# Performance work log

Measured on AMD Instinct MI355X. Metric: run time of the kernel, lower is better.

Reference implementation:

```python
import jax, jax.numpy as jnp
import numpy as np

N_WAY = 5
N_SHOT = 10

def setup_inputs() -> dict:
    key = jax.random.key(0)
    k1, k2, k3, k4 = jax.random.split(key, 4)
    B, n_support, n_query, T, F, D = 32, 50, 75, 128, 64, 256
    support_x = jax.random.normal(k1, (B, n_support, T, F), dtype=jnp.float32)
    query_x = jax.random.normal(k2, (B, n_query, T, F), dtype=jnp.float32)
    # episodic labels: every class present exactly N_SHOT times per episode
    support_y = jnp.broadcast_to(jnp.repeat(jnp.arange(N_WAY), N_SHOT)[None, :], (B, n_support))
    W = jax.random.normal(k3, (F, D), dtype=jnp.float32) * 0.05
    b = jax.random.normal(k4, (D,), dtype=jnp.float32) * 0.05
    return {"support_x": support_x, "support_y": support_y, "query_x": query_x, "W": W, "b": b}

def _encode(x, W, b):
    # mean-pool over time, then linear projection: [B, N, T, F] -> [B, N, D]
    return jnp.einsum('bntf,fd->bnd', x, W) / x.shape[2] + b

def reference(support_x, support_y, query_x, W, b):
    B, n_query = query_x.shape[0], query_x.shape[1]
    support_z = _encode(support_x, W, b)   # [B, S, D]
    query_z = _encode(query_x, W, b)       # [B, Q, D]
    # label-grouped mean (prototypes) via one-hot segment sum, all episodes at once
    onehot = (support_y[..., None] == jnp.arange(N_WAY)).astype(support_z.dtype)  # [B, S, K]
    counts = onehot.sum(axis=1)                                                   # [B, K]
    prototypes = jnp.einsum('bsk,bsd->bkd', onehot, support_z) / counts[..., None]
    # Euclidean cdist: [B, Q, K]
    diff = query_z[:, :, None, :] - prototypes[:, None, :, :]
    dists = jnp.sqrt(jnp.sum(diff * diff, axis=-1))
    logits = -dists
    return logits.reshape(B * n_query, N_WAY)
```

## Files before the change

### kernel.cpp

```cpp
#include <hip/hip_runtime.h>
#include <math.h>

#define B_  32
#define NS_ 50
#define NQ_ 75
#define T_  128
#define F_  64
#define D_  256
#define K_  5
#define NR_ (NS_ + NQ_)
#define QT_ 25

__global__ __launch_bounds__(256) void meanpool_kernel(
    const float* __restrict__ sx, const float* __restrict__ qx,
    float* __restrict__ meanbuf)
{
    const int bid = blockIdx.x;
    const int b = bid / NR_, n = bid % NR_;
    const float* src = (n < NS_)
        ? (sx + (size_t)(b * NS_ + n) * (T_ * F_))
        : (qx + (size_t)(b * NQ_ + (n - NS_)) * (T_ * F_));
    const float4* src4 = (const float4*)src;

    const int tid = threadIdx.x;
    const int f4 = tid & 15;

    float4 acc = make_float4(0.f, 0.f, 0.f, 0.f);
    for (int t = (tid >> 4); t < T_; t += 16) {
        float4 v = src4[t * 16 + f4];
        acc.x += v.x; acc.y += v.y; acc.z += v.z; acc.w += v.w;
    }
    acc.x += __shfl_down(acc.x, 32); acc.y += __shfl_down(acc.y, 32);
    acc.z += __shfl_down(acc.z, 32); acc.w += __shfl_down(acc.w, 32);
    acc.x += __shfl_down(acc.x, 16); acc.y += __shfl_down(acc.y, 16);
    acc.z += __shfl_down(acc.z, 16); acc.w += __shfl_down(acc.w, 16);

    __shared__ float4 red[4][16];
    const int wave = tid >> 6, lane = tid & 63;
    if (lane < 16) red[wave][lane] = acc;
    __syncthreads();
    if (tid < 16) {
        float4 a = red[0][tid], b4 = red[1][tid], c = red[2][tid], d4 = red[3][tid];
        float4 s;
        s.x = (a.x + b4.x + c.x + d4.x) * (1.f / T_);
        s.y = (a.y + b4.y + c.y + d4.y) * (1.f / T_);
        s.z = (a.z + b4.z + c.z + d4.z) * (1.f / T_);
        s.w = (a.w + b4.w + c.w + d4.w) * (1.f / T_);
        ((float4*)meanbuf)[(size_t)bid * 16 + tid] = s;
    }
}

__global__ __launch_bounds__(256) void proto_kernel(
    const float* __restrict__ meanbuf, const int* __restrict__ sy,
    const float* __restrict__ Wm, const float* __restrict__ bias,
    float* __restrict__ out)
{
    __shared__ float rows[QT_ + K_][F_];
    __shared__ float zbuf[QT_ + K_][D_];
    __shared__ int   labels[NS_];
    __shared__ float psum[K_][F_];
    __shared__ int   counts[K_];

    const int tid = threadIdx.x;
    const int bid = blockIdx.x;
    const int b = bid / 3, qt = bid % 3;
    const int q0 = qt * QT_;

    if (tid < NS_) labels[tid] = sy[b * NS_ + tid];
    __syncthreads();

    if (tid < F_) {
        const int f = tid;
        float p0 = 0.f, p1 = 0.f, p2 = 0.f, p3 = 0.f, p4 = 0.f;
        for (int s = 0; s < NS_; ++s) {
            float v = meanbuf[((size_t)b * NR_ + s) * F_ + f];
            int l = labels[s];
            if      (l == 0) p0 += v;
            else if (l == 1) p1 += v;
            else if (l == 2) p2 += v;
            else if (l == 3) p3 += v;
            else             p4 += v;
        }
        psum[0][f] = p0; psum[1][f] = p1; psum[2][f] = p2;
        psum[3][f] = p3; psum[4][f] = p4;
    }
    if (tid < K_) {
        int c = 0;
        for (int s = 0; s < NS_; ++s) c += (labels[s] == tid);
        counts[tid] = c;
    }
    for (int i = tid; i < QT_ * F_; i += 256) {
        int r = i / F_, f = i % F_;
        rows[r][f] = meanbuf[((size_t)b * NR_ + NS_ + q0 + r) * F_ + f];
    }
    __syncthreads();
    for (int i = tid; i < K_ * F_; i += 256) {
        int k = i / F_, f = i % F_;
        rows[QT_ + k][f] = psum[k][f] / (float)counts[k];
    }
    __syncthreads();

    {
        const int d = tid;
        float wreg[F_];
#pragma unroll
        for (int f = 0; f < F_; ++f) wreg[f] = Wm[f * D_ + d];
        const float bd = bias[d];
        for (int r = 0; r < QT_ + K_; ++r) {
            float acc = bd;
#pragma unroll
            for (int f = 0; f < F_; ++f) acc += rows[r][f] * wreg[f];
            zbuf[r][d] = acc;
        }
    }
    __syncthreads();

    const int wave = tid >> 6, lane = tid & 63;
    for (int p = wave; p < QT_ * K_; p += 4) {
        const int q = p / K_, k = p % K_;
        float s = 0.f;
#pragma unroll
        for (int j = 0; j < 4; ++j) {
            int d = lane + j * 64;
            float diff = zbuf[q][d] - zbuf[QT_ + k][d];
            s += diff * diff;
        }
        for (int off = 32; off > 0; off >>= 1) s += __shfl_down(s, off);
        if (lane == 0) out[(size_t)(b * NQ_ + q0 + q) * K_ + k] = -sqrtf(s);
    }
}

extern "C" void kernel_launch(void* const* d_in, const int* in_sizes, int n_in,
                              void* d_out, int out_size, void* d_ws, size_t ws_size,
                              hipStream_t stream) {
    const float* sx   = (const float*)d_in[0];
    const int*   sy   = (const int*)  d_in[1];
    const float* qx   = (const float*)d_in[2];
    const float* Wm   = (const float*)d_in[3];
    const float* bias = (const float*)d_in[4];
    float* out = (float*)d_out;
    float* meanbuf = (float*)d_ws;

    meanpool_kernel<<<B_ * NR_, 256, 0, stream>>>(sx, qx, meanbuf);
    proto_kernel<<<B_ * 3, 256, 0, stream>>>(meanbuf, sy, Wm, bias, out);
}
```

Measured before the change: 202.8 us.

## Fuse linear projection into mean-pool kernel and simplify distance kernel

Moves the F-to-D projection out of the small 96-block second kernel and into the 4000-block mean-pool kernel, so each encoded row is projected once right after pooling. The second kernel now only builds prototypes from projected support rows and computes distances. The time loop is also fully unrolled. In exchange, every pooling block loads the full 64-float weight column per thread, which adds register pressure and weight reads, and the workspace grows from D=64 to D=256 floats per row.

```diff
diff --git a/kernel.cpp b/kernel.cpp
--- a/kernel.cpp
+++ b/kernel.cpp
@@ -11,9 +11,10 @@
 #define NR_ (NS_ + NQ_)
 #define QT_ 25
 
-__global__ __launch_bounds__(256) void meanpool_kernel(
+__global__ __launch_bounds__(256) void encode_kernel(
     const float* __restrict__ sx, const float* __restrict__ qx,
-    float* __restrict__ meanbuf)
+    const float* __restrict__ Wm, const float* __restrict__ bias,
+    float* __restrict__ zbuf)
 {
     const int bid = blockIdx.x;
     const int b = bid / NR_, n = bid % NR_;
@@ -23,10 +24,17 @@
     const float4* src4 = (const float4*)src;
 
     const int tid = threadIdx.x;
+
+    float wreg[F_];
+#pragma unroll
+    for (int f = 0; f < F_; ++f) wreg[f] = Wm[f * D_ + tid];
+    const float bd = bias[tid];
+
     const int f4 = tid & 15;
-
     float4 acc = make_float4(0.f, 0.f, 0.f, 0.f);
-    for (int t = (tid >> 4); t < T_; t += 16) {
+#pragma unroll
+    for (int j = 0; j < 8; ++j) {
+        int t = (tid >> 4) + j * 16;
         float4 v = src4[t * 16 + f4];
         acc.x += v.x; acc.y += v.y; acc.z += v.z; acc.w += v.w;
     }
@@ -36,6 +44,7 @@
     acc.z += __shfl_down(acc.z, 16); acc.w += __shfl_down(acc.w, 16);
 
     __shared__ float4 red[4][16];
+    __shared__ float  mean[F_];
     const int wave = tid >> 6, lane = tid & 63;
     if (lane < 16) red[wave][lane] = acc;
     __syncthreads();
@@ -46,20 +55,27 @@
         s.y = (a.y + b4.y + c.y + d4.y) * (1.f / T_);
         s.z = (a.z + b4.z + c.z + d4.z) * (1.f / T_);
         s.w = (a.w + b4.w + c.w + d4.w) * (1.f / T_);
-        ((float4*)meanbuf)[(size_t)bid * 16 + tid] = s;
+        ((float4*)mean)[tid] = s;
     }
+    __syncthreads();
+
+    float z = bd;
+    const float2* m2 = (const float2*)mean;
+#pragma unroll
+    for (int f2 = 0; f2 < F_ / 2; ++f2) {
+        float2 mv = m2[f2];
+        z += mv.x * wreg[2 * f2] + mv.y * wreg[2 * f2 + 1];
+    }
+    zbuf[(size_t)bid * D_ + tid] = z;
 }
 
-__global__ __launch_bounds__(256) void proto_kernel(
-    const float* __restrict__ meanbuf, const int* __restrict__ sy,
-    const float* __restrict__ Wm, const float* __restrict__ bias,
+__global__ __launch_bounds__(256) void dist_kernel(
+    const float* __restrict__ zbuf, const int* __restrict__ sy,
     float* __restrict__ out)
 {
-    __shared__ float rows[QT_ + K_][F_];
-    __shared__ float zbuf[QT_ + K_][D_];
+    __shared__ float zq[QT_][D_];
+    __shared__ float proto[K_][D_];
     __shared__ int   labels[NS_];
-    __shared__ float psum[K_][F_];
-    __shared__ int   counts[K_];
 
     const int tid = threadIdx.x;
     const int bid = blockIdx.x;
@@ -69,50 +85,27 @@
     if (tid < NS_) labels[tid] = sy[b * NS_ + tid];
     __syncthreads();
 
-    if (tid < F_) {
-        const int f = tid;
+    {
         float p0 = 0.f, p1 = 0.f, p2 = 0.f, p3 = 0.f, p4 = 0.f;
+        int   c0 = 0, c1 = 0, c2 = 0, c3 = 0, c4 = 0;
         for (int s = 0; s < NS_; ++s) {
-            float v = meanbuf[((size_t)b * NR_ + s) * F_ + f];
+            float v = zbuf[((size_t)b * NR_ + s) * D_ + tid];
             int l = labels[s];
-            if      (l == 0) p0 += v;
-            else if (l == 1) p1 += v;
-            else if (l == 2) p2 += v;
-            else if (l == 3) p3 += v;
-            else             p4 += v;
+            if      (l == 0) { p0 += v; ++c0; }
+            else if (l == 1) { p1 += v; ++c1; }
+            else if (l == 2) { p2 += v; ++c2; }
+            else if (l == 3) { p3 += v; ++c3; }
+            else             { p4 += v; ++c4; }
         }
-        psum[0][f] = p0; psum[1][f] = p1; psum[2][f] = p2;
-        psum[3][f] = p3; psum[4][f] = p4;
+        proto[0][tid] = p0 / (float)c0;
+        proto[1][tid] = p1 / (float)c1;
+        proto[2][tid] = p2 / (float)c2;
+        proto[3][tid] = p3 / (float)c3;
+        proto[4][tid] = p4 / (float)c4;
     }
-    if (tid < K_) {
-        int c = 0;
-        for (int s = 0; s < NS_; ++s) c += (labels[s] == tid);
-        counts[tid] = c;
-    }
-    for (int i = tid; i < QT_ * F_; i += 256) {
-        int r = i / F_, f = i % F_;
-        rows[r][f] = meanbuf[((size_t)b * NR_ + NS_ + q0 + r) * F_ + f];
-    }
-    __syncthreads();
-    for (int i = tid; i < K_ * F_; i += 256) {
-        int k = i / F_, f = i % F_;
-        rows[QT_ + k][f] = psum[k][f] / (float)counts[k];
-    }
-    __syncthreads();
-
-    {
-        const int d = tid;
-        float wreg[F_];
 #pragma unroll
-        for (int f = 0; f < F_; ++f) wreg[f] = Wm[f * D_ + d];
-        const float bd = bias[d];
-        for (int r = 0; r < QT_ + K_; ++r) {
-            float acc = bd;
-#pragma unroll
-            for (int f = 0; f < F_; ++f) acc += rows[r][f] * wreg[f];
-            zbuf[r][d] = acc;
-        }
-    }
+    for (int j = 0; j < QT_; ++j)
+        zq[j][tid] = zbuf[((size_t)b * NR_ + NS_ + q0 + j) * D_ + tid];
     __syncthreads();
 
     const int wave = tid >> 6, lane = tid & 63;
@@ -122,7 +115,7 @@
 #pragma unroll
         for (int j = 0; j < 4; ++j) {
             int d = lane + j * 64;
-            float diff = zbuf[q][d] - zbuf[QT_ + k][d];
+            float diff = zq[q][d] - proto[k][d];
             s += diff * diff;
         }
         for (int off = 32; off > 0; off >>= 1) s += __shfl_down(s, off);
@@ -139,8 +132,8 @@
     const float* Wm   = (const float*)d_in[3];
     const float* bias = (const float*)d_in[4];
     float* out = (float*)d_out;
-    float* meanbuf = (float*)d_ws;
+    float* zbuf = (float*)d_ws;
 
-    meanpool_kernel<<<B_ * NR_, 256, 0, stream>>>(sx, qx, meanbuf);
-    proto_kernel<<<B_ * 3, 256, 0, stream>>>(meanbuf, sy, Wm, bias, out);
+    encode_kernel<<<B_ * NR_, 256, 0, stream>>>(sx, qx, Wm, bias, zbuf);
+    dist_kernel<<<B_ * 3, 256, 0, stream>>>(zbuf, sy, out);
 }
```

New measurement: 187.7 us. 1.08x faster.
